# Kernel optimization log

Hardware: AMD Instinct MI355X
Metric: run time of the kernel (lower is better)

The kernel has to match this reference:

```python
import jax, jax.numpy as jnp
import numpy as np

EPS = 1e-08


def setup_inputs() -> dict:
    key = jax.random.key(0)
    k1, k2 = jax.random.split(key)
    B, K, H = 8, 8000, 512
    inputs = jax.random.normal(k1, (B, K, H), dtype=jnp.float32)
    gamma = jax.random.normal(k2, (1, H), dtype=jnp.float32) * 0.05  # 'random_normal' init
    beta = jnp.zeros((1, H), dtype=jnp.float32)
    return {"inputs": inputs, "gamma": gamma, "beta": beta}


def reference(inputs, gamma, beta):
    # Cumulative (causal) layer norm: at step k, normalize frame k using
    # mean/var computed over the prefix inputs[:, :k+1, :] (time and feature dims).
    B, K, H = inputs.shape
    # Running sums over time of per-frame sums across features -> O(K) scan.
    step_sum = jnp.sum(inputs, axis=-1)          # [B, K]
    step_sumsq = jnp.sum(inputs * inputs, axis=-1)  # [B, K]
    cum_sum = jnp.cumsum(step_sum, axis=1)       # [B, K]
    cum_sumsq = jnp.cumsum(step_sumsq, axis=1)   # [B, K]
    count = (jnp.arange(1, K + 1, dtype=inputs.dtype) * H)  # [K] elements in each prefix
    mean = cum_sum / count                        # [B, K]
    var = cum_sumsq / count - mean * mean         # [B, K]
    inv_std = 1.0 / jnp.sqrt(var + EPS)           # matches (var + eps) ** 0.5
    # gamma/beta: (1, H) broadcast over [B, K, H]
    out = gamma * ((inputs - mean[..., None]) * inv_std[..., None]) + beta
    return out
```

## Files before the change

### kernel.cpp

```cpp
#include <hip/hip_runtime.h>
#include <math.h>


#define HDIM 512
#define F4H (HDIM / 4)
#define SEG 64
#define BATCHES 8

typedef float f32x4 __attribute__((ext_vector_type(4)));

__global__ __launch_bounds__(256) void k_seg_sums(
    const float* __restrict__ in, float* __restrict__ ssum,
    float* __restrict__ ssq, double* __restrict__ segS,
    double* __restrict__ segQ, int K, int segsPerBatch)
{
    const int lane = threadIdx.x & 63;
    const int wid  = threadIdx.x >> 6;
    const int segGlobal = blockIdx.x;
    const int b   = segGlobal / segsPerBatch;
    const int seg = segGlobal % segsPerBatch;
    const int k0  = seg * SEG;

    double accS = 0.0, accQ = 0.0;
    #pragma unroll 4
    for (int i = 0; i < SEG / 4; ++i) {
        const int fk = k0 + wid * (SEG / 4) + i;
        if (fk < K) {
            const float4* p = (const float4*)in + ((size_t)b * K + fk) * F4H;
            float4 a = p[lane];
            float4 c = p[lane + 64];
            float s = (a.x + a.y) + (a.z + a.w) + (c.x + c.y) + (c.z + c.w);
            float q = (a.x * a.x + a.y * a.y) + (a.z * a.z + a.w * a.w)
                    + (c.x * c.x + c.y * c.y) + (c.z * c.z + c.w * c.w);
            #pragma unroll
            for (int off = 32; off >= 1; off >>= 1) {
                s += __shfl_xor(s, off);
                q += __shfl_xor(q, off);
            }
            if (lane == 0) {
                ssum[(size_t)b * K + fk] = s;
                ssq[(size_t)b * K + fk]  = q;
            }
            accS += (double)s;
            accQ += (double)q;
        }
    }
    __shared__ double wS[4], wQ[4];
    if (lane == 0) { wS[wid] = accS; wQ[wid] = accQ; }
    __syncthreads();
    if (threadIdx.x == 0) {
        segS[segGlobal] = wS[0] + wS[1] + wS[2] + wS[3];
        segQ[segGlobal] = wQ[0] + wQ[1] + wQ[2] + wQ[3];
    }
}

__global__ __launch_bounds__(256) void k_norm_fused(
    const float* __restrict__ in, const float* __restrict__ gamma,
    const float* __restrict__ beta, const float* __restrict__ ssum,
    const float* __restrict__ ssq, const double* __restrict__ segS,
    const double* __restrict__ segQ, float* __restrict__ out,
    int K, int segsPerBatch)
{
    __shared__ float meanS[SEG], istdS[SEG];

    const int tid  = threadIdx.x;
    const int lane = tid & 63;
    const int wid  = tid >> 6;
    const int segGlobal = blockIdx.x;
    const int b = segGlobal / segsPerBatch;
    const int s = segGlobal % segsPerBatch;
    const int k0 = s * SEG;

    const f32x4 g0  = ((const f32x4*)gamma)[lane];
    const f32x4 g1  = ((const f32x4*)gamma)[lane + 64];
    const f32x4 be0 = ((const f32x4*)beta)[lane];
    const f32x4 be1 = ((const f32x4*)beta)[lane + 64];

    if (wid == 0) {
        double es = 0.0, eq = 0.0;
        for (int base = 0; base < s; base += 64) {
            const int j = base + lane;
            if (j < s) {
                es += segS[(size_t)b * segsPerBatch + j];
                eq += segQ[(size_t)b * segsPerBatch + j];
            }
        }
        #pragma unroll
        for (int off = 32; off >= 1; off >>= 1) {
            es += __shfl_xor(es, off);
            eq += __shfl_xor(eq, off);
        }
        const int k = k0 + lane;
        double sc = 0.0, qc = 0.0;
        if (k < K) {
            sc = (double)ssum[(size_t)b * K + k];
            qc = (double)ssq[(size_t)b * K + k];
        }
        #pragma unroll
        for (int off = 1; off < 64; off <<= 1) {
            double s2 = __shfl_up(sc, off);
            double q2 = __shfl_up(qc, off);
            if (lane >= off) { sc += s2; qc += q2; }
        }
        sc += es; qc += eq;
        if (k < K) {
            const double cnt = (double)(k + 1) * (double)HDIM;
            const double m   = sc / cnt;
            const double var = qc / cnt - m * m;
            meanS[lane] = (float)m;
            istdS[lane] = (float)(1.0 / sqrt(var + 1e-8));
        }
    }
    __syncthreads();

    #pragma unroll 4
    for (int i = 0; i < SEG / 4; ++i) {
        const int fi = wid * (SEG / 4) + i;
        const int k = k0 + fi;
        if (k < K) {
            const f32x4* p = (const f32x4*)in + ((size_t)b * K + k) * F4H;
            const f32x4 a = p[lane];
            const f32x4 c = p[lane + 64];
            const float m = meanS[fi];
            const float r = istdS[fi];
            f32x4 o0, o1;
            o0.x = g0.x * ((a.x - m) * r) + be0.x;
            o0.y = g0.y * ((a.y - m) * r) + be0.y;
            o0.z = g0.z * ((a.z - m) * r) + be0.z;
            o0.w = g0.w * ((a.w - m) * r) + be0.w;
            o1.x = g1.x * ((c.x - m) * r) + be1.x;
            o1.y = g1.y * ((c.y - m) * r) + be1.y;
            o1.z = g1.z * ((c.z - m) * r) + be1.z;
            o1.w = g1.w * ((c.w - m) * r) + be1.w;
            f32x4* q = (f32x4*)out + ((size_t)b * K + k) * F4H;
            __builtin_nontemporal_store(o0, q + lane);
            __builtin_nontemporal_store(o1, q + lane + 64);
        }
    }
}

extern "C" void kernel_launch(void* const* d_in, const int* in_sizes, int n_in,
                              void* d_out, int out_size, void* d_ws, size_t ws_size,
                              hipStream_t stream)
{
    const float* in    = (const float*)d_in[0];
    const float* gamma = (const float*)d_in[1];
    const float* beta  = (const float*)d_in[2];
    float* out = (float*)d_out;

    const int H = in_sizes[1];
    const int BK = in_sizes[0] / H;
    const int K = BK / BATCHES;
    const int segsPerBatch = (K + SEG - 1) / SEG;
    const int NSEG = BATCHES * segsPerBatch;
    (void)H; (void)n_in; (void)out_size; (void)ws_size;

    float* ssum = (float*)d_ws;
    float* ssq  = ssum + BK;
    double* segS = (double*)(ssq + BK);
    double* segQ = segS + NSEG;

    k_seg_sums<<<dim3(NSEG), dim3(256), 0, stream>>>(
        in, ssum, ssq, segS, segQ, K, segsPerBatch);
    k_norm_fused<<<dim3(NSEG), dim3(256), 0, stream>>>(
        in, gamma, beta, ssum, ssq, segS, segQ, out, K, segsPerBatch);
}
```

Baseline: 67.13 us.

## Fuse segment-sum and normalize passes into one persistent kernel with grid barrier

Replaces the two-kernel pipeline with a single kernel where each block computes its segment sums, publishes them via atomics, spin-waits on a per-batch counter until all segments are done, then normalizes. Part of the input tile is held in LDS and registers so only half the frames are re-read from global memory, and the second launch is gone. The approach relies on all 1000 blocks being co-resident (checked via occupancy query) and adds a memset plus spin-wait cost; the fallback keeps the old path.

```diff
diff --git a/kernel.cpp b/kernel.cpp
--- a/kernel.cpp
+++ b/kernel.cpp
@@ -6,8 +6,148 @@
 #define F4H (HDIM / 4)
 #define SEG 64
 #define BATCHES 8
+#define KLEN 8000
+#define SEGS (KLEN / SEG)
+#define NBLK (BATCHES * SEGS)
 
 typedef float f32x4 __attribute__((ext_vector_type(4)));
+typedef unsigned long long u64;
+
+__global__ __launch_bounds__(256, 4) void cln_fused1(
+    const float* __restrict__ in, const float* __restrict__ gamma,
+    const float* __restrict__ beta, float* __restrict__ out,
+    double* __restrict__ segS, double* __restrict__ segQ,
+    unsigned int* __restrict__ done)
+{
+    __shared__ f32x4 stage[16][F4H];
+    __shared__ float fsum[SEG], fsq[SEG], meanS[SEG], istdS[SEG];
+    __shared__ double wS[4], wQ[4];
+
+    const int tid  = threadIdx.x;
+    const int lane = tid & 63;
+    const int wid  = tid >> 6;
+    const int bx   = blockIdx.x;
+    const int b    = bx / SEGS;
+    const int s    = bx % SEGS;
+    const int k0   = s * SEG;
+
+    const f32x4 g0  = ((const f32x4*)gamma)[lane];
+    const f32x4 g1  = ((const f32x4*)gamma)[lane + 64];
+    const f32x4 be0 = ((const f32x4*)beta)[lane];
+    const f32x4 be1 = ((const f32x4*)beta)[lane + 64];
+
+    const f32x4* p = (const f32x4*)in + ((size_t)b * KLEN + k0 + wid * 16) * F4H;
+
+    f32x4 xa[4], xc[4];
+    double accS = 0.0, accQ = 0.0;
+    #pragma unroll
+    for (int fi = 0; fi < 16; ++fi) {
+        const f32x4 a = p[(size_t)fi * F4H + lane];
+        const f32x4 c = p[(size_t)fi * F4H + 64 + lane];
+        float sv = (a.x + a.y) + (a.z + a.w) + (c.x + c.y) + (c.z + c.w);
+        float qv = (a.x * a.x + a.y * a.y) + (a.z * a.z + a.w * a.w)
+                 + (c.x * c.x + c.y * c.y) + (c.z * c.z + c.w * c.w);
+        #pragma unroll
+        for (int off = 32; off >= 1; off >>= 1) {
+            sv += __shfl_xor(sv, off);
+            qv += __shfl_xor(qv, off);
+        }
+        if (lane == 0) { fsum[wid * 16 + fi] = sv; fsq[wid * 16 + fi] = qv; }
+        accS += (double)sv;
+        accQ += (double)qv;
+        if (fi < 4) {
+            stage[wid * 4 + fi][lane]      = a;
+            stage[wid * 4 + fi][64 + lane] = c;
+        } else if (fi < 8) {
+            xa[fi - 4] = a; xc[fi - 4] = c;
+        }
+    }
+    if (lane == 0) { wS[wid] = accS; wQ[wid] = accQ; }
+    __syncthreads();
+    if (tid == 0) {
+        const double S = wS[0] + wS[1] + wS[2] + wS[3];
+        const double Q = wQ[0] + wQ[1] + wQ[2] + wQ[3];
+        __hip_atomic_store((u64*)&segS[bx], __double_as_longlong(S),
+                           __ATOMIC_RELAXED, __HIP_MEMORY_SCOPE_AGENT);
+        __hip_atomic_store((u64*)&segQ[bx], __double_as_longlong(Q),
+                           __ATOMIC_RELAXED, __HIP_MEMORY_SCOPE_AGENT);
+        __hip_atomic_fetch_add(&done[b], 1u,
+                               __ATOMIC_RELEASE, __HIP_MEMORY_SCOPE_AGENT);
+        while (__hip_atomic_load(&done[b], __ATOMIC_ACQUIRE,
+                                 __HIP_MEMORY_SCOPE_AGENT) < (unsigned)SEGS)
+            __builtin_amdgcn_s_sleep(32);
+    }
+    __syncthreads();
+
+    if (wid == 0) {
+        double es = 0.0, eq = 0.0;
+        for (int base = 0; base < s; base += 64) {
+            const int j = base + lane;
+            if (j < s) {
+                es += __longlong_as_double(__hip_atomic_load(
+                        (u64*)&segS[b * SEGS + j],
+                        __ATOMIC_RELAXED, __HIP_MEMORY_SCOPE_AGENT));
+                eq += __longlong_as_double(__hip_atomic_load(
+                        (u64*)&segQ[b * SEGS + j],
+                        __ATOMIC_RELAXED, __HIP_MEMORY_SCOPE_AGENT));
+            }
+        }
+        #pragma unroll
+        for (int off = 32; off >= 1; off >>= 1) {
+            es += __shfl_xor(es, off);
+            eq += __shfl_xor(eq, off);
+        }
+        double sc = (double)fsum[lane], qc = (double)fsq[lane];
+        #pragma unroll
+        for (int off = 1; off < 64; off <<= 1) {
+            double s2 = __shfl_up(sc, off);
+            double q2 = __shfl_up(qc, off);
+            if (lane >= off) { sc += s2; qc += q2; }
+        }
+        sc += es; qc += eq;
+        const double cnt = (double)(k0 + lane + 1) * (double)HDIM;
+        const double m   = sc / cnt;
+        const double var = qc / cnt - m * m;
+        meanS[lane] = (float)m;
+        istdS[lane] = (float)(1.0 / sqrt(var + 1e-8));
+    }
+    __syncthreads();
+
+    f32x4* o4 = (f32x4*)out + ((size_t)b * KLEN + k0 + wid * 16) * F4H;
+
+#define APPLY(fi, a, c) {                                                   \
+        const float m = meanS[wid * 16 + (fi)];                             \
+        const float r = istdS[wid * 16 + (fi)];                             \
+        f32x4 o0, o1;                                                       \
+        o0.x = g0.x * ((a.x - m) * r) + be0.x;                              \
+        o0.y = g0.y * ((a.y - m) * r) + be0.y;                              \
+        o0.z = g0.z * ((a.z - m) * r) + be0.z;                              \
+        o0.w = g0.w * ((a.w - m) * r) + be0.w;                              \
+        o1.x = g1.x * ((c.x - m) * r) + be1.x;                              \
+        o1.y = g1.y * ((c.y - m) * r) + be1.y;                              \
+        o1.z = g1.z * ((c.z - m) * r) + be1.z;                              \
+        o1.w = g1.w * ((c.w - m) * r) + be1.w;                              \
+        __builtin_nontemporal_store(o0, o4 + (size_t)(fi) * F4H + lane);    \
+        __builtin_nontemporal_store(o1, o4 + (size_t)(fi) * F4H + 64 + lane); }
+
+    #pragma unroll
+    for (int fi = 8; fi < 16; ++fi) {
+        const f32x4 a = p[(size_t)fi * F4H + lane];
+        const f32x4 c = p[(size_t)fi * F4H + 64 + lane];
+        APPLY(fi, a, c);
+    }
+    #pragma unroll
+    for (int fi = 4; fi < 8; ++fi) {
+        APPLY(fi, xa[fi - 4], xc[fi - 4]);
+    }
+    #pragma unroll
+    for (int fi = 0; fi < 4; ++fi) {
+        const f32x4 a = stage[wid * 4 + fi][lane];
+        const f32x4 c = stage[wid * 4 + fi][64 + lane];
+        APPLY(fi, a, c);
+    }
+#undef APPLY
+}
 
 __global__ __launch_bounds__(256) void k_seg_sums(
     const float* __restrict__ in, float* __restrict__ ssum,
@@ -66,9 +206,8 @@
     const int tid  = threadIdx.x;
     const int lane = tid & 63;
     const int wid  = tid >> 6;
-    const int segGlobal = blockIdx.x;
-    const int b = segGlobal / segsPerBatch;
-    const int s = segGlobal % segsPerBatch;
+    const int b = blockIdx.x / segsPerBatch;
+    const int s = blockIdx.x % segsPerBatch;
     const int k0 = s * SEG;
 
     const f32x4 g0  = ((const f32x4*)gamma)[lane];
@@ -153,15 +292,34 @@
     const int K = BK / BATCHES;
     const int segsPerBatch = (K + SEG - 1) / SEG;
     const int NSEG = BATCHES * segsPerBatch;
-    (void)H; (void)n_in; (void)out_size; (void)ws_size;
-
-    float* ssum = (float*)d_ws;
+    (void)n_in; (void)out_size; (void)ws_size;
+
+    double* segS = (double*)d_ws;
+    double* segQ = segS + NSEG;
+    unsigned int* done = (unsigned int*)(segQ + NSEG);
+    float* ssum = (float*)(done + 16);
     float* ssq  = ssum + BK;
-    double* segS = (double*)(ssq + BK);
-    double* segQ = segS + NSEG;
-
-    k_seg_sums<<<dim3(NSEG), dim3(256), 0, stream>>>(
-        in, ssum, ssq, segS, segQ, K, segsPerBatch);
-    k_norm_fused<<<dim3(NSEG), dim3(256), 0, stream>>>(
-        in, gamma, beta, ssum, ssq, segS, segQ, out, K, segsPerBatch);
+
+    bool fused = (H == HDIM) && (K == KLEN) && (BK == BATCHES * KLEN);
+    if (fused) {
+        int dev = 0, nb = 0, cus = 0;
+        if (hipGetDevice(&dev) != hipSuccess) fused = false;
+        if (fused && hipOccupancyMaxActiveBlocksPerMultiprocessor(
+                        &nb, (const void*)cln_fused1, 256, 0) != hipSuccess)
+            fused = false;
+        if (fused && hipDeviceGetAttribute(&cus, hipDeviceAttributeMultiprocessorCount,
+                                           dev) != hipSuccess) fused = false;
+        if (fused && (long)nb * cus < NBLK) fused = false;
+    }
+
+    if (fused) {
+        hipMemsetAsync(done, 0, 16 * sizeof(unsigned int), stream);
+        cln_fused1<<<dim3(NBLK), dim3(256), 0, stream>>>(
+            in, gamma, beta, out, segS, segQ, done);
+    } else {
+        k_seg_sums<<<dim3(NSEG), dim3(256), 0, stream>>>(
+            in, ssum, ssq, segS, segQ, K, segsPerBatch);
+        k_norm_fused<<<dim3(NSEG), dim3(256), 0, stream>>>(
+            in, gamma, beta, ssum, ssq, segS, segQ, out, K, segsPerBatch);
+    }
 }
```

After: 66.95 us. No clear change (-0.3%).
